# Kernel tuning notes

Measured on AMD Instinct MI355X. Metric: run time of the kernel, lower is better.

Reference implementation:

```python
import jax, jax.numpy as jnp
import numpy as np

EPS = 1e-5
SLOPE = 0.2


def _ico_conv(x, neigh, w, b):
    # x: (B, C, N); neigh: (N, 7) -> gather 1-ring, flatten channel-major, linear
    g = x[:, :, neigh]                          # (B, C, N, 7)
    B, C, N, K = g.shape
    g = g.transpose(0, 2, 1, 3).reshape(B, N, C * K)
    y = jnp.einsum('bnf,of->bno', g, w) + b     # (B, N, out)
    return y.transpose(0, 2, 1)                 # (B, out, N)


def _bn(x, gamma, beta):
    # BatchNorm1d with track_running_stats=False: batch stats over (B, N)
    mean = x.mean(axis=(0, 2), keepdims=True)
    var = x.var(axis=(0, 2), keepdims=True)
    xhat = (x - mean) * jax.lax.rsqrt(var + EPS)
    return xhat * gamma[None, :, None] + beta[None, :, None]


def _lrelu(x):
    return jnp.where(x >= 0, x, SLOPE * x)


def setup_inputs() -> dict:
    key = jax.random.key(0)
    ks = jax.random.split(key, 10)
    B, IN_CH, OUT_CH = 2, 128, 64
    N_DOWN, N_UP, K = 40962, 163842, 7
    inp = {
        'x1': jax.random.normal(ks[0], (B, IN_CH, N_DOWN), jnp.float32),
        'x2': jax.random.normal(ks[1], (B, OUT_CH, N_UP), jnp.float32),
        'up_fc_w': jax.random.normal(ks[2], (OUT_CH, IN_CH), jnp.float32) * 0.05,
        'up_fc_b': jax.random.normal(ks[3], (OUT_CH,), jnp.float32) * 0.05,
        'conv1_w': jax.random.normal(ks[4], (OUT_CH, K * IN_CH), jnp.float32) * 0.05,
        'conv1_b': jax.random.normal(ks[5], (OUT_CH,), jnp.float32) * 0.05,
        'bn1_g': jnp.ones((OUT_CH,), jnp.float32),
        'bn1_b': jnp.zeros((OUT_CH,), jnp.float32),
        'conv2_w': jax.random.normal(ks[6], (OUT_CH, K * OUT_CH), jnp.float32) * 0.05,
        'conv2_b': jax.random.normal(ks[7], (OUT_CH,), jnp.float32) * 0.05,
        'bn2_g': jnp.ones((OUT_CH,), jnp.float32),
        'bn2_b': jnp.zeros((OUT_CH,), jnp.float32),
        'up_neigh': jax.random.randint(ks[8], (N_UP, 2), 0, N_DOWN, jnp.int32),
        'conv_neigh': jax.random.randint(ks[9], (N_UP, K), 0, N_UP, jnp.int32),
        'max_pool_indices': jnp.zeros((1,), jnp.int32),  # unused for up_mode='interp'
    }
    return inp


def reference(x1, x2, up_fc_w, up_fc_b, conv1_w, conv1_b, bn1_g, bn1_b,
              conv2_w, conv2_b, bn2_g, bn2_b, up_neigh, conv_neigh,
              max_pool_indices):
    # --- IcoUpSampleLayer ('interp'): Linear(in->out) then 2-neighbor mean ---
    h = jnp.einsum('bcn,oc->bno', x1, up_fc_w) + up_fc_b   # (B, N_down, out)
    h = h[:, up_neigh].mean(axis=2)                        # (B, N_up, out)
    x1_up = h.transpose(0, 2, 1)                           # (B, out, N_up)
    # --- concat skip along channels ---
    x = jnp.concatenate([x1_up, x2], axis=1)               # (B, in_ch, N_up)
    # --- (conv => BN => LeakyReLU) * 2 ---
    x = _lrelu(_bn(_ico_conv(x, conv_neigh, conv1_w, conv1_b), bn1_g, bn1_b))
    x = _lrelu(_bn(_ico_conv(x, conv_neigh, conv2_w, conv2_b), bn2_g, bn2_b))
    return x
```

## Files before the change

kernel.cpp:

```cpp
#include <hip/hip_runtime.h>
#include <hip/hip_bf16.h>

typedef __hip_bfloat16 bf16;
typedef short bf16x8 __attribute__((ext_vector_type(8)));
typedef float f32x4 __attribute__((ext_vector_type(4)));

#define ND     40962
#define NUP    163842
#define NBATCH 2
#define NT     2561
#define BN_EPS 1e-5
#define SLOPE  0.2f

#define OFF_W1P   0ull
#define OFF_W2P   114688ull
#define OFF_STATS 172032ull
#define OFF_H     173056ull
#define OFF_P2    (OFF_H + 2622464ull)
#define OFF_XCAT  10659328ull
#define OFF_Y     94546432ull

__device__ __forceinline__ void gload_lds16(const void* g, void* l) {
  __builtin_amdgcn_global_load_lds(
      (const __attribute__((address_space(1))) void*)g,
      (__attribute__((address_space(3))) void*)l, 16, 0, 0);
}

__device__ __forceinline__ float lrelu(float v) { return v >= 0.0f ? v : SLOPE * v; }

__global__ __launch_bounds__(256) void k_permw(const float* __restrict__ w1,
                                               const float* __restrict__ w2,
                                               bf16* __restrict__ w1p, bf16* __restrict__ w2p) {
  int t = blockIdx.x * 256 + threadIdx.x;
  if (t < 64 * 896) {
    int o = t / 896, f = t % 896;
    int kk = f / 128, c = f % 128;
    w1p[t] = __float2bfloat16(w1[o * 896 + c * 7 + kk]);
  } else if (t < 64 * 896 + 64 * 448) {
    int idx = t - 64 * 896;
    int o = idx / 448, f = idx % 448;
    int kk = f / 64, c = f % 64;
    w2p[idx] = __float2bfloat16(w2[o * 448 + c * 7 + kk]);
  }
}

__global__ __launch_bounds__(256) void k_h(const float* __restrict__ x1,
                                           const float* __restrict__ wfc,
                                           const float* __restrict__ bfc,
                                           bf16* __restrict__ h) {
  __shared__ float wl[128 * 64];
  __shared__ float bl[64];
  int tid = threadIdx.x, b = blockIdx.y;
  for (int i = tid; i < 8192; i += 256) { int o = i >> 7, c = i & 127; wl[c * 64 + o] = wfc[i]; }
  if (tid < 64) bl[tid] = bfc[tid];
  __syncthreads();
  int n = blockIdx.x * 256 + tid;
  int nc = n < ND ? n : ND - 1;
  float acc[64];
#pragma unroll
  for (int o = 0; o < 64; ++o) acc[o] = bl[o];
#pragma unroll 4
  for (int c = 0; c < 128; ++c) {
    float xv = x1[((size_t)b * 128 + c) * (size_t)ND + nc];
    const f32x4* wrow = (const f32x4*)(wl + c * 64);
#pragma unroll
    for (int og = 0; og < 16; ++og) {
      f32x4 wv = wrow[og];
      acc[og * 4 + 0] = fmaf(xv, wv[0], acc[og * 4 + 0]);
      acc[og * 4 + 1] = fmaf(xv, wv[1], acc[og * 4 + 1]);
      acc[og * 4 + 2] = fmaf(xv, wv[2], acc[og * 4 + 2]);
      acc[og * 4 + 3] = fmaf(xv, wv[3], acc[og * 4 + 3]);
    }
  }
  if (n < ND) {
    bf16* hp = h + ((size_t)b * ND + n) * 64;
#pragma unroll
    for (int og = 0; og < 8; ++og) {
      union { bf16x8 v; bf16 e[8]; } u;
#pragma unroll
      for (int j = 0; j < 8; ++j) u.e[j] = __float2bfloat16(acc[og * 8 + j]);
      ((bf16x8*)hp)[og] = u.v;
    }
  }
}

__global__ __launch_bounds__(256) void k_xcat(const float* __restrict__ x2,
                                              const bf16* __restrict__ h,
                                              const int* __restrict__ upn,
                                              bf16* __restrict__ xcat) {
  __shared__ float tt[64][65];
  __shared__ int un[64][2];
  int tid = threadIdx.x, b = blockIdx.y;
  int m0 = blockIdx.x * 64;
#pragma unroll
  for (int i = 0; i < 16; ++i) {
    int c = i * 4 + (tid >> 6);
    int ml = tid & 63;
    int m = m0 + ml; if (m >= NUP) m = NUP - 1;
    tt[c][ml] = x2[((size_t)b * 64 + c) * (size_t)NUP + m];
  }
  if (tid < 128) {
    int ml = tid >> 1, w = tid & 1;
    int m = m0 + ml; if (m >= NUP) m = NUP - 1;
    un[ml][w] = upn[(size_t)m * 2 + w];
  }
  __syncthreads();
  int ln = tid >> 2, p = tid & 3;
  int m = m0 + ln;
  if (m >= NUP) return;
  bf16* dst = xcat + ((size_t)b * NUP + m) * 128;
  if (p < 2) {
    int c0 = p * 32;
    const bf16* h0 = h + ((size_t)b * ND + un[ln][0]) * 64 + c0;
    const bf16* h1 = h + ((size_t)b * ND + un[ln][1]) * 64 + c0;
#pragma unroll
    for (int q = 0; q < 4; ++q) {
      union { bf16x8 v; bf16 e[8]; } a, bb, o_;
      a.v = ((const bf16x8*)h0)[q];
      bb.v = ((const bf16x8*)h1)[q];
#pragma unroll
      for (int j = 0; j < 8; ++j)
        o_.e[j] = __float2bfloat16(0.5f * (__bfloat162float(a.e[j]) + __bfloat162float(bb.e[j])));
      ((bf16x8*)(dst + c0))[q] = o_.v;
    }
  } else {
    int c0 = (p - 2) * 32;
#pragma unroll
    for (int q = 0; q < 4; ++q) {
      union { bf16x8 v; bf16 e[8]; } o_;
#pragma unroll
      for (int j = 0; j < 8; ++j) o_.e[j] = __float2bfloat16(tt[c0 + q * 8 + j][ln]);
      ((bf16x8*)(dst + 64 + c0))[q] = o_.v;
    }
  }
}

template <int CIN>
__global__ __launch_bounds__(256) void k_conv(const bf16* __restrict__ x,
                                              const int* __restrict__ neigh,
                                              const bf16* __restrict__ wp,
                                              const float* __restrict__ bias,
                                              float* __restrict__ y,
                                              float* __restrict__ partials) {
  constexpr int CHA = CIN / 8;
  __shared__ bf16 lA[64 * CIN];
  __shared__ bf16 lW[64 * CIN];
  __shared__ int nb_[64 * 7];
  __shared__ float lred[4][2][64];
  int tid = threadIdx.x, b = blockIdx.y;
  int n0 = blockIdx.x * 64;
  int wv = tid >> 6, lane = tid & 63;

  for (int i = tid; i < 448; i += 256) {
    int nd = n0 + i / 7; if (nd >= NUP) nd = NUP - 1;
    nb_[i] = neigh[(size_t)nd * 7 + i % 7];
  }
  f32x4 acc[4];
#pragma unroll
  for (int ot = 0; ot < 4; ++ot) {
    float bv = bias[ot * 16 + (lane & 15)];
    acc[ot] = (f32x4){bv, bv, bv, bv};
  }
  __syncthreads();

  const bf16* xb = x + (size_t)b * NUP * CIN;
  for (int kk = 0; kk < 7; ++kk) {
#pragma unroll
    for (int i = 0; i < (64 * CHA) / 256; ++i) {
      int lin = i * 256 + tid;
      int row = lin / CHA, slot = lin % CHA;
      int gs = slot ^ (row & 7);
      int node = nb_[row * 7 + kk];
      gload_lds16(xb + (size_t)node * CIN + gs * 8, lA + (size_t)(i * 256 + wv * 64) * 8);
    }
#pragma unroll
    for (int i = 0; i < (64 * CHA) / 256; ++i) {
      int lin = i * 256 + tid;
      int o = lin / CHA, slot = lin % CHA;
      int gs = slot ^ (o & 7);
      gload_lds16(wp + (size_t)o * (7 * CIN) + kk * CIN + gs * 8,
                  lW + (size_t)(i * 256 + wv * 64) * 8);
    }
    __syncthreads();
#pragma unroll
    for (int ks = 0; ks < CIN / 32; ++ks) {
      int r = wv * 16 + (lane & 15);
      int g0 = ks * 4 + (lane >> 4);
      bf16x8 a = *(const bf16x8*)(lA + (size_t)(r * CHA + (g0 ^ (r & 7))) * 8);
#pragma unroll
      for (int ot = 0; ot < 4; ++ot) {
        int o = ot * 16 + (lane & 15);
        bf16x8 bb = *(const bf16x8*)(lW + (size_t)(o * CHA + (g0 ^ (o & 7))) * 8);
        acc[ot] = __builtin_amdgcn_mfma_f32_16x16x32_bf16(a, bb, acc[ot], 0, 0, 0);
      }
    }
    __syncthreads();
  }

  float s[4], q[4];
#pragma unroll
  for (int ot = 0; ot < 4; ++ot) {
    s[ot] = 0.0f; q[ot] = 0.0f;
    int o = ot * 16 + (lane & 15);
#pragma unroll
    for (int i = 0; i < 4; ++i) {
      int node = n0 + wv * 16 + (lane >> 4) * 4 + i;
      float v = acc[ot][i];
      if (node < NUP) {
        y[((size_t)b * NUP + node) * 64 + o] = v;
        s[ot] += v; q[ot] += v * v;
      }
    }
  }
#pragma unroll
  for (int ot = 0; ot < 4; ++ot) {
    s[ot] += __shfl_xor(s[ot], 16); s[ot] += __shfl_xor(s[ot], 32);
    q[ot] += __shfl_xor(q[ot], 16); q[ot] += __shfl_xor(q[ot], 32);
  }
  if (lane < 16) {
#pragma unroll
    for (int ot = 0; ot < 4; ++ot) {
      lred[wv][0][ot * 16 + lane] = s[ot];
      lred[wv][1][ot * 16 + lane] = q[ot];
    }
  }
  __syncthreads();
  if (tid < 128) {
    int which = tid >> 6, c = tid & 63;
    float p = lred[0][which][c] + lred[1][which][c] + lred[2][which][c] + lred[3][which][c];
    partials[((size_t)b * gridDim.x + blockIdx.x) * 128 + which * 64 + c] = p;
  }
}

__global__ __launch_bounds__(256) void k_red1(const float* __restrict__ p, int nblk,
                                              float* __restrict__ p2) {
  int g = blockIdx.x * 2 + threadIdx.x / 128;
  int j = threadIdx.x & 127;
  float a = 0.0f;
  for (int r = g; r < nblk; r += 128) a += p[(size_t)r * 128 + j];
  p2[(size_t)g * 128 + j] = a;
}

__global__ __launch_bounds__(128) void k_stats(const float* __restrict__ p2,
                                               const float* __restrict__ g,
                                               const float* __restrict__ be,
                                               float* __restrict__ sc, float* __restrict__ sh) {
  __shared__ double red[128];
  int j = threadIdx.x;
  double a = 0.0;
  for (int r = 0; r < 128; ++r) a += (double)p2[r * 128 + j];
  red[j] = a;
  __syncthreads();
  if (j < 64) {
    double M = (double)NBATCH * (double)NUP;
    double mean = red[j] / M;
    double var = red[64 + j] / M - mean * mean;
    float s = g[j] * (float)(1.0 / sqrt(var + BN_EPS));
    sc[j] = s;
    sh[j] = be[j] - (float)mean * s;
  }
}

__global__ __launch_bounds__(256) void k_bnapply(const float* __restrict__ y,
                                                 const float* __restrict__ sc,
                                                 const float* __restrict__ sh,
                                                 bf16* __restrict__ z) {
  __shared__ float ssc[64], ssh[64];
  int tid = threadIdx.x;
  if (tid < 64) { ssc[tid] = sc[tid]; ssh[tid] = sh[tid]; }
  __syncthreads();
  size_t e = ((size_t)blockIdx.x * 256 + tid) * 8;
  if (e >= (size_t)NBATCH * NUP * 64) return;
  int c0 = (int)(e & 63);
  f32x4 v0 = *(const f32x4*)(y + e);
  f32x4 v1 = *(const f32x4*)(y + e + 4);
  float vv[8] = {v0[0], v0[1], v0[2], v0[3], v1[0], v1[1], v1[2], v1[3]};
  union { bf16x8 v; bf16 el[8]; } o_;
#pragma unroll
  for (int j = 0; j < 8; ++j) {
    float zz = lrelu(fmaf(vv[j], ssc[c0 + j], ssh[c0 + j]));
    o_.el[j] = __float2bfloat16(zz);
  }
  *(bf16x8*)(z + e) = o_.v;
}

__global__ __launch_bounds__(256) void k_final(const float* __restrict__ y,
                                               const float* __restrict__ sc,
                                               const float* __restrict__ sh,
                                               float* __restrict__ out) {
  __shared__ float t[64][65];
  __shared__ float ssc[64], ssh[64];
  int tid = threadIdx.x, b = blockIdx.y;
  int n0 = blockIdx.x * 64;
  if (tid < 64) { ssc[tid] = sc[tid]; ssh[tid] = sh[tid]; }
  __syncthreads();
#pragma unroll
  for (int i = 0; i < 16; ++i) {
    int lin = i * 256 + tid;
    int nl = lin >> 6, c = lin & 63;
    int n = n0 + nl;
    float v = 0.0f;
    if (n < NUP) v = y[((size_t)b * NUP + n) * 64 + c];
    t[nl][c] = lrelu(fmaf(v, ssc[c], ssh[c]));
  }
  __syncthreads();
#pragma unroll
  for (int i = 0; i < 16; ++i) {
    int lin = i * 256 + tid;
    int c = lin >> 6, nl = lin & 63;
    int n = n0 + nl;
    if (n < NUP) out[((size_t)b * 64 + c) * (size_t)NUP + n] = t[nl][c];
  }
}

extern "C" void kernel_launch(void* const* d_in, const int* in_sizes, int n_in,
                              void* d_out, int out_size, void* d_ws, size_t ws_size,
                              hipStream_t stream) {
  const float* x1      = (const float*)d_in[0];
  const float* x2      = (const float*)d_in[1];
  const float* up_fc_w = (const float*)d_in[2];
  const float* up_fc_b = (const float*)d_in[3];
  const float* conv1_w = (const float*)d_in[4];
  const float* conv1_b = (const float*)d_in[5];
  const float* bn1_g   = (const float*)d_in[6];
  const float* bn1_b   = (const float*)d_in[7];
  const float* conv2_w = (const float*)d_in[8];
  const float* conv2_b = (const float*)d_in[9];
  const float* bn2_g   = (const float*)d_in[10];
  const float* bn2_b   = (const float*)d_in[11];
  const int* up_neigh  = (const int*)d_in[12];
  const int* conv_nei  = (const int*)d_in[13];

  char* ws = (char*)d_ws;
  bf16*  w1p  = (bf16*)(ws + OFF_W1P);
  bf16*  w2p  = (bf16*)(ws + OFF_W2P);
  float* sc   = (float*)(ws + OFF_STATS);
  float* sh   = sc + 64;
  bf16*  h    = (bf16*)(ws + OFF_H);
  float* part = (float*)(ws + OFF_H);
  float* p2   = (float*)(ws + OFF_P2);
  bf16*  xcat = (bf16*)(ws + OFF_XCAT);
  bf16*  z1   = (bf16*)(ws + OFF_XCAT);
  float* y    = (float*)(ws + OFF_Y);
  float* out  = (float*)d_out;

  k_permw<<<336, 256, 0, stream>>>(conv1_w, conv2_w, w1p, w2p);
  k_h<<<dim3(161, 2), 256, 0, stream>>>(x1, up_fc_w, up_fc_b, h);
  k_xcat<<<dim3(NT, 2), 256, 0, stream>>>(x2, h, up_neigh, xcat);
  k_conv<128><<<dim3(NT, 2), 256, 0, stream>>>(xcat, conv_nei, w1p, conv1_b, y, part);
  k_red1<<<64, 256, 0, stream>>>(part, 2 * NT, p2);
  k_stats<<<1, 128, 0, stream>>>(p2, bn1_g, bn1_b, sc, sh);
  k_bnapply<<<10241, 256, 0, stream>>>(y, sc, sh, z1);
  k_conv<64><<<dim3(NT, 2), 256, 0, stream>>>(z1, conv_nei, w2p, conv2_b, y, part);
  k_red1<<<64, 256, 0, stream>>>(part, 2 * NT, p2);
  k_stats<<<1, 128, 0, stream>>>(p2, bn2_g, bn2_b, sc, sh);
  k_final<<<dim3(NT, 2), 256, 0, stream>>>(y, sc, sh, out);
}
```

Before: 356.3 us.

## Load conv operands directly to registers, enlarge node tile, store pre-BN output in bf16

```diff
diff --git a/kernel.cpp b/kernel.cpp
--- a/kernel.cpp
+++ b/kernel.cpp
@@ -8,7 +8,8 @@
 #define ND     40962
 #define NUP    163842
 #define NBATCH 2
-#define NT     2561
+#define NTC    641
+#define NT64   2561
 #define BN_EPS 1e-5
 #define SLOPE  0.2f
 
@@ -19,12 +20,6 @@
 #define OFF_P2    (OFF_H + 2622464ull)
 #define OFF_XCAT  10659328ull
 #define OFF_Y     94546432ull
-
-__device__ __forceinline__ void gload_lds16(const void* g, void* l) {
-  __builtin_amdgcn_global_load_lds(
-      (const __attribute__((address_space(1))) void*)g,
-      (__attribute__((address_space(3))) void*)l, 16, 0, 0);
-}
 
 __device__ __forceinline__ float lrelu(float v) { return v >= 0.0f ? v : SLOPE * v; }
 
@@ -140,75 +135,74 @@
                                               const int* __restrict__ neigh,
                                               const bf16* __restrict__ wp,
                                               const float* __restrict__ bias,
-                                              float* __restrict__ y,
+                                              bf16* __restrict__ y,
                                               float* __restrict__ partials) {
-  constexpr int CHA = CIN / 8;
-  __shared__ bf16 lA[64 * CIN];
-  __shared__ bf16 lW[64 * CIN];
-  __shared__ int nb_[64 * 7];
+  __shared__ int nbl[4 * 448];
   __shared__ float lred[4][2][64];
   int tid = threadIdx.x, b = blockIdx.y;
-  int n0 = blockIdx.x * 64;
+  int n0 = blockIdx.x * 256;
   int wv = tid >> 6, lane = tid & 63;
-
-  for (int i = tid; i < 448; i += 256) {
-    int nd = n0 + i / 7; if (nd >= NUP) nd = NUP - 1;
-    nb_[i] = neigh[(size_t)nd * 7 + i % 7];
-  }
-  f32x4 acc[4];
+  int l15 = lane & 15, l4 = lane >> 4;
+
+  for (int j = lane; j < 448; j += 64) {
+    int gi = (n0 + wv * 64) * 7 + j;
+    int gmax = NUP * 7 - 1;
+    nbl[wv * 448 + j] = neigh[gi <= gmax ? gi : gmax];
+  }
+
+  f32x4 acc[4][4];
 #pragma unroll
   for (int ot = 0; ot < 4; ++ot) {
-    float bv = bias[ot * 16 + (lane & 15)];
-    acc[ot] = (f32x4){bv, bv, bv, bv};
-  }
-  __syncthreads();
+    float bv = bias[ot * 16 + l15];
+#pragma unroll
+    for (int rg = 0; rg < 4; ++rg) acc[rg][ot] = (f32x4){bv, bv, bv, bv};
+  }
 
   const bf16* xb = x + (size_t)b * NUP * CIN;
+  const int coff = l4 * 8;
+  const int bo = l15 * (7 * CIN) + coff;
+
   for (int kk = 0; kk < 7; ++kk) {
-#pragma unroll
-    for (int i = 0; i < (64 * CHA) / 256; ++i) {
-      int lin = i * 256 + tid;
-      int row = lin / CHA, slot = lin % CHA;
-      int gs = slot ^ (row & 7);
-      int node = nb_[row * 7 + kk];
-      gload_lds16(xb + (size_t)node * CIN + gs * 8, lA + (size_t)(i * 256 + wv * 64) * 8);
-    }
-#pragma unroll
-    for (int i = 0; i < (64 * CHA) / 256; ++i) {
-      int lin = i * 256 + tid;
-      int o = lin / CHA, slot = lin % CHA;
-      int gs = slot ^ (o & 7);
-      gload_lds16(wp + (size_t)o * (7 * CIN) + kk * CIN + gs * 8,
-                  lW + (size_t)(i * 256 + wv * 64) * 8);
-    }
-    __syncthreads();
+    int nd[4];
+#pragma unroll
+    for (int rg = 0; rg < 4; ++rg)
+      nd[rg] = nbl[wv * 448 + (rg * 16 + l15) * 7 + kk];
+    const bf16* wk = wp + kk * CIN;
 #pragma unroll
     for (int ks = 0; ks < CIN / 32; ++ks) {
-      int r = wv * 16 + (lane & 15);
-      int g0 = ks * 4 + (lane >> 4);
-      bf16x8 a = *(const bf16x8*)(lA + (size_t)(r * CHA + (g0 ^ (r & 7))) * 8);
+      bf16x8 a[4], bbf[4];
+#pragma unroll
+      for (int rg = 0; rg < 4; ++rg)
+        a[rg] = *(const bf16x8*)(xb + (size_t)nd[rg] * CIN + ks * 32 + coff);
+#pragma unroll
+      for (int ot = 0; ot < 4; ++ot)
+        bbf[ot] = *(const bf16x8*)(wk + bo + ot * (16 * 7 * CIN) + ks * 32);
+#pragma unroll
+      for (int ot = 0; ot < 4; ++ot)
+#pragma unroll
+        for (int rg = 0; rg < 4; ++rg)
+          acc[rg][ot] = __builtin_amdgcn_mfma_f32_16x16x32_bf16(a[rg], bbf[ot], acc[rg][ot], 0, 0, 0);
+    }
+  }
+
+  float s[4], q[4];
+#pragma unroll
+  for (int ot = 0; ot < 4; ++ot) { s[ot] = 0.0f; q[ot] = 0.0f; }
+  bf16* yb = y + (size_t)b * NUP * 64;
+#pragma unroll
+  for (int rg = 0; rg < 4; ++rg) {
+    int nodebase = n0 + wv * 64 + rg * 16 + l4 * 4;
+#pragma unroll
+    for (int i = 0; i < 4; ++i) {
+      int node = nodebase + i;
+      bool ok = node < NUP;
 #pragma unroll
       for (int ot = 0; ot < 4; ++ot) {
-        int o = ot * 16 + (lane & 15);
-        bf16x8 bb = *(const bf16x8*)(lW + (size_t)(o * CHA + (g0 ^ (o & 7))) * 8);
-        acc[ot] = __builtin_amdgcn_mfma_f32_16x16x32_bf16(a, bb, acc[ot], 0, 0, 0);
-      }
-    }
-    __syncthreads();
-  }
-
-  float s[4], q[4];
-#pragma unroll
-  for (int ot = 0; ot < 4; ++ot) {
-    s[ot] = 0.0f; q[ot] = 0.0f;
-    int o = ot * 16 + (lane & 15);
-#pragma unroll
-    for (int i = 0; i < 4; ++i) {
-      int node = n0 + wv * 16 + (lane >> 4) * 4 + i;
-      float v = acc[ot][i];
-      if (node < NUP) {
-        y[((size_t)b * NUP + node) * 64 + o] = v;
-        s[ot] += v; q[ot] += v * v;
+        float v = acc[rg][ot][i];
+        if (ok) {
+          yb[(size_t)node * 64 + ot * 16 + l15] = __float2bfloat16(v);
+          s[ot] += v; q[ot] += v * v;
+        }
       }
     }
   }
@@ -261,7 +255,7 @@
   }
 }
 
-__global__ __launch_bounds__(256) void k_bnapply(const float* __restrict__ y,
+__global__ __launch_bounds__(256) void k_bnapply(const bf16* __restrict__ y,
                                                  const float* __restrict__ sc,
                                                  const float* __restrict__ sh,
                                                  bf16* __restrict__ z) {
@@ -272,19 +266,17 @@
   size_t e = ((size_t)blockIdx.x * 256 + tid) * 8;
   if (e >= (size_t)NBATCH * NUP * 64) return;
   int c0 = (int)(e & 63);
-  f32x4 v0 = *(const f32x4*)(y + e);
-  f32x4 v1 = *(const f32x4*)(y + e + 4);
-  float vv[8] = {v0[0], v0[1], v0[2], v0[3], v1[0], v1[1], v1[2], v1[3]};
-  union { bf16x8 v; bf16 el[8]; } o_;
+  union { bf16x8 v; bf16 el[8]; } in_, o_;
+  in_.v = *(const bf16x8*)(y + e);
 #pragma unroll
   for (int j = 0; j < 8; ++j) {
-    float zz = lrelu(fmaf(vv[j], ssc[c0 + j], ssh[c0 + j]));
-    o_.el[j] = __float2bfloat16(zz);
+    float f = __bfloat162float(in_.el[j]);
+    o_.el[j] = __float2bfloat16(lrelu(fmaf(f, ssc[c0 + j], ssh[c0 + j])));
   }
   *(bf16x8*)(z + e) = o_.v;
 }
 
-__global__ __launch_bounds__(256) void k_final(const float* __restrict__ y,
+__global__ __launch_bounds__(256) void k_final(const bf16* __restrict__ y,
                                                const float* __restrict__ sc,
                                                const float* __restrict__ sh,
                                                float* __restrict__ out) {
@@ -294,22 +286,30 @@
   int n0 = blockIdx.x * 64;
   if (tid < 64) { ssc[tid] = sc[tid]; ssh[tid] = sh[tid]; }
   __syncthreads();
+  int ln = tid >> 2, qc = tid & 3;
+  int n = n0 + ln; if (n >= NUP) n = NUP - 1;
+  const bf16* yp = y + ((size_t)b * NUP + n) * 64 + qc * 16;
+  union { bf16x8 v; bf16 el[8]; } v0, v1;
+  v0.v = ((const bf16x8*)yp)[0];
+  v1.v = ((const bf16x8*)yp)[1];
+#pragma unroll
+  for (int j = 0; j < 8; ++j) {
+    int c = qc * 16 + j;
+    t[ln][c] = lrelu(fmaf(__bfloat162float(v0.el[j]), ssc[c], ssh[c]));
+  }
+#pragma unroll
+  for (int j = 0; j < 8; ++j) {
+    int c = qc * 16 + 8 + j;
+    t[ln][c] = lrelu(fmaf(__bfloat162float(v1.el[j]), ssc[c], ssh[c]));
+  }
+  __syncthreads();
+  int nl = tid & 63;
+  int nn = n0 + nl;
+  if (nn >= NUP) return;
 #pragma unroll
   for (int i = 0; i < 16; ++i) {
-    int lin = i * 256 + tid;
-    int nl = lin >> 6, c = lin & 63;
-    int n = n0 + nl;
-    float v = 0.0f;
-    if (n < NUP) v = y[((size_t)b * NUP + n) * 64 + c];
-    t[nl][c] = lrelu(fmaf(v, ssc[c], ssh[c]));
-  }
-  __syncthreads();
-#pragma unroll
-  for (int i = 0; i < 16; ++i) {
-    int lin = i * 256 + tid;
-    int c = lin >> 6, nl = lin & 63;
-    int n = n0 + nl;
-    if (n < NUP) out[((size_t)b * 64 + c) * (size_t)NUP + n] = t[nl][c];
+    int c = i * 4 + (tid >> 6);
+    out[((size_t)b * 64 + c) * (size_t)NUP + nn] = t[nl][c];
   }
 }
 
@@ -341,18 +341,18 @@
   float* p2   = (float*)(ws + OFF_P2);
   bf16*  xcat = (bf16*)(ws + OFF_XCAT);
   bf16*  z1   = (bf16*)(ws + OFF_XCAT);
-  float* y    = (float*)(ws + OFF_Y);
+  bf16*  y    = (bf16*)(ws + OFF_Y);
   float* out  = (float*)d_out;
 
   k_permw<<<336, 256, 0, stream>>>(conv1_w, conv2_w, w1p, w2p);
   k_h<<<dim3(161, 2), 256, 0, stream>>>(x1, up_fc_w, up_fc_b, h);
-  k_xcat<<<dim3(NT, 2), 256, 0, stream>>>(x2, h, up_neigh, xcat);
-  k_conv<128><<<dim3(NT, 2), 256, 0, stream>>>(xcat, conv_nei, w1p, conv1_b, y, part);
-  k_red1<<<64, 256, 0, stream>>>(part, 2 * NT, p2);
+  k_xcat<<<dim3(NT64, 2), 256, 0, stream>>>(x2, h, up_neigh, xcat);
+  k_conv<128><<<dim3(NTC, 2), 256, 0, stream>>>(xcat, conv_nei, w1p, conv1_b, y, part);
+  k_red1<<<64, 256, 0, stream>>>(part, 2 * NTC, p2);
   k_stats<<<1, 128, 0, stream>>>(p2, bn1_g, bn1_b, sc, sh);
   k_bnapply<<<10241, 256, 0, stream>>>(y, sc, sh, z1);
-  k_conv<64><<<dim3(NT, 2), 256, 0, stream>>>(z1, conv_nei, w2p, conv2_b, y, part);
-  k_red1<<<64, 256, 0, stream>>>(part, 2 * NT, p2);
+  k_conv<64><<<dim3(NTC, 2), 256, 0, stream>>>(z1, conv_nei, w2p, conv2_b, y, part);
+  k_red1<<<64, 256, 0, stream>>>(part, 2 * NTC, p2);
   k_stats<<<1, 128, 0, stream>>>(p2, bn2_g, bn2_b, sc, sh);
-  k_final<<<dim3(NT, 2), 256, 0, stream>>>(y, sc, sh, out);
-}
+  k_final<<<dim3(NT64, 2), 256, 0, stream>>>(y, sc, sh, out);
+}
```

Result: slower. 436.2 us (+22.4%).
